# Kernel optimization log

Hardware: AMD Instinct MI355X
Metric: run time of the kernel (lower is better)

The kernel has to match this reference:

```python
import jax, jax.numpy as jnp
import numpy as np

N_E = 8192
E_DIM = 64
BETA = 0.25
N_TOKENS = 32768


def setup_inputs() -> dict:
    key = jax.random.key(0)
    k1, k2 = jax.random.split(key)
    x = jax.random.normal(k1, (N_TOKENS, E_DIM), dtype=jnp.float32)
    # nn.Embedding weight initialized uniform(-1/n_e, 1/n_e)
    codebook = jax.random.uniform(k2, (N_E, E_DIM), dtype=jnp.float32,
                                  minval=-1.0 / N_E, maxval=1.0 / N_E)
    return {"x": x, "codebook": codebook, "start": 0, "end": N_E, "use_sk": 0}


def reference(x, codebook, start, end, use_sk):
    # use_sk=0 -> argmin branch (sinkhorn branch calls external helper, not exercised)
    latent = x.reshape(-1, E_DIM)                       # [N, D]
    cb = codebook[start:end]                            # [K, D]
    # squared euclidean distances: ||z||^2 + ||e||^2 - 2 z.e
    d = (jnp.sum(latent * latent, axis=1, keepdims=True)
         + jnp.sum(cb * cb, axis=1)[None, :]
         - 2.0 * jnp.einsum('nd,kd->nk', latent, cb))   # [N, K]
    indices = jnp.argmin(d, axis=-1) + start            # [N]
    x_q = codebook[indices].reshape(x.shape)            # gather
    sg = jax.lax.stop_gradient
    commitment_loss = jnp.mean((sg(x_q) - x) ** 2)
    codebook_loss = jnp.mean((x_q - sg(x)) ** 2)
    loss = codebook_loss + BETA * commitment_loss
    x_q_st = x + sg(x_q - x)                            # straight-through estimator
    indices = indices.reshape(x.shape[:-1])
    return x_q_st, loss, indices
```

## Files before the change

kernel.cpp:

```cpp
#include <hip/hip_runtime.h>
#include <math.h>


#define N_E    8192
#define EDIM   64
#define NTOK   32768
#define NELEM  (NTOK * EDIM)
#define CSZ    32
#define NCHUNK (N_E / CSZ)
#define WINDOW 3e-4f
#define KEXT   80
#define TTOK   256
#define TCODE  2048
#define SROW   88

typedef __attribute__((ext_vector_type(8)))  short          short8;
typedef __attribute__((ext_vector_type(8)))  unsigned short ushort8v;
typedef __attribute__((ext_vector_type(4)))  unsigned short ushort4v;
typedef __attribute__((ext_vector_type(16))) float          f32x16;

__device__ __forceinline__ unsigned short f2bf(float f) {
  unsigned int u = __float_as_uint(f);
  return (unsigned short)((u + 0x7FFFu + ((u >> 16) & 1u)) >> 16);
}
__device__ __forceinline__ unsigned short f2h(float f) {
  union { _Float16 h; unsigned short u; } cv; cv.h = (_Float16)f; return cv.u;
}
__device__ __forceinline__ float h2f(unsigned short b) {
  union { _Float16 h; unsigned short u; } cv; cv.u = b; return (float)cv.h;
}

__global__ __launch_bounds__(256) void vq_sc(const float* __restrict__ cb,
                                             float* __restrict__ sc,
                                             unsigned short* __restrict__ cbf) {
#pragma clang fp contract(off)
  int r = blockIdx.x * 256 + threadIdx.x;
  const float4* c4 = (const float4*)(cb + (size_t)r * EDIM);
  float a[8];
#pragma unroll
  for (int j = 0; j < 8; ++j) a[j] = 0.0f;
#pragma unroll
  for (int i = 0; i < 8; ++i) {
    float4 pA = c4[2*i], pB = c4[2*i+1];
    a[0] += pA.x * pA.x; a[1] += pA.y * pA.y; a[2] += pA.z * pA.z; a[3] += pA.w * pA.w;
    a[4] += pB.x * pB.x; a[5] += pB.y * pB.y; a[6] += pB.z * pB.z; a[7] += pB.w * pB.w;
  }
  float sval = ((a[0]+a[1]) + (a[2]+a[3])) + ((a[4]+a[5]) + (a[6]+a[7]));
  sc[r] = sval;
  unsigned short* dst = cbf + (size_t)r * KEXT;
#pragma unroll
  for (int h = 0; h < 8; ++h) {
    float4 fA = c4[2*h], fB = c4[2*h+1];
    ushort8v o = {f2bf(fA.x), f2bf(fA.y), f2bf(fA.z), f2bf(fA.w),
                  f2bf(fB.x), f2bf(fB.y), f2bf(fB.z), f2bf(fB.w)};
    *(ushort8v*)&dst[h * 8] = o;
  }
  ushort8v t0 = {0,0,0,0,0,0,0,0};
  t0[0] = f2bf(sval);
  *(ushort8v*)&dst[64] = t0;
  ushort8v z = {0,0,0,0,0,0,0,0};
  *(ushort8v*)&dst[72] = z;
}

__global__ __launch_bounds__(256, 2) void vq_pass1(
    const float* __restrict__ x, const unsigned short* __restrict__ cbf,
    unsigned short* __restrict__ minima, unsigned int* __restrict__ maskb,
    const int* __restrict__ p_start, const int* __restrict__ p_end) {
  __shared__ unsigned short Xs[TTOK * SROW];
  __shared__ unsigned short Cs[128 * SROW];
  int tid = threadIdx.x;
  int tb = blockIdx.x;
  int cbk = blockIdx.y;
  int s = *p_start, e = *p_end;

  const float4* xg = (const float4*)(x + (size_t)tb * TTOK * EDIM);
#pragma unroll
  for (int p = 0; p < 16; ++p) {
    int idx = tid + p * 256;
    int row = idx >> 4, c4i = idx & 15;
    float4 f = xg[idx];
    ushort4v o = {f2bf(f.x), f2bf(f.y), f2bf(f.z), f2bf(f.w)};
    *(ushort4v*)&Xs[row * SROW + c4i * 4] = o;
  }
  {
    ushort8v t0 = {0,0,0,0,0,0,0,0};
    t0[0] = f2bf(-0.5f);
    ushort8v z = {0,0,0,0,0,0,0,0};
    *(ushort8v*)&Xs[tid * SROW + 64] = t0;
    *(ushort8v*)&Xs[tid * SROW + 72] = z;
  }
  const ushort8v* cg0 = (const ushort8v*)(cbf + (size_t)cbk * TCODE * KEXT);
#pragma unroll
  for (int p = 0; p < 5; ++p) {
    int idx = tid + p * 256;
    int row = idx / 10, h = idx % 10;
    *(ushort8v*)&Cs[row * SROW + h * 8] = cg0[idx];
  }
  __syncthreads();

  int lane = tid & 63, wv = tid >> 6;
  int half = lane >> 5, ln = lane & 31;
  int tokbase = wv * 64;
  short8 bfr[2][5];
#pragma unroll
  for (int tg = 0; tg < 2; ++tg)
#pragma unroll
    for (int ks = 0; ks < 5; ++ks)
      bfr[tg][ks] = *(const short8*)&Xs[(tokbase + tg*32 + ln) * SROW + ks*16 + half*8];

  for (int nb = 0; nb < 16; ++nb) {
    ushort8v creg[5];
    if (nb < 15) {
      const ushort8v* cg =
          (const ushort8v*)(cbf + ((size_t)cbk * TCODE + (nb + 1) * 128) * KEXT);
#pragma unroll
      for (int p = 0; p < 5; ++p) creg[p] = cg[tid + p * 256];
    }
    f32x16 acc[2][4];
#pragma unroll
    for (int tg = 0; tg < 2; ++tg)
#pragma unroll
      for (int ct = 0; ct < 4; ++ct) acc[tg][ct] = (f32x16)0.0f;
#pragma unroll
    for (int ks = 0; ks < 5; ++ks)
#pragma unroll
      for (int ct = 0; ct < 4; ++ct) {
        short8 a = *(const short8*)&Cs[(ct*32 + ln) * SROW + ks*16 + half*8];
        acc[0][ct] = __builtin_amdgcn_mfma_f32_32x32x16_bf16(a, bfr[0][ks],
                                                             acc[0][ct], 0, 0, 0);
        acc[1][ct] = __builtin_amdgcn_mfma_f32_32x32x16_bf16(a, bfr[1][ks],
                                                             acc[1][ct], 0, 0, 0);
      }
    __syncthreads();
    if (nb < 15) {
#pragma unroll
      for (int p = 0; p < 5; ++p) {
        int idx = tid + p * 256;
        int row = idx / 10, h = idx % 10;
        *(ushort8v*)&Cs[row * SROW + h * 8] = creg[p];
      }
    }
    int cbase0 = cbk * TCODE + nb * 128;
    float vmv[2][4];
    unsigned mbits[2][4];
#pragma unroll
    for (int ct = 0; ct < 4; ++ct) {
      int c0 = cbase0 + ct * 32;
      bool full = (c0 >= s) && (c0 + 32 <= e);
#pragma unroll
      for (int tg = 0; tg < 2; ++tg) {
        float v = -INFINITY;
        if (full) {
#pragma unroll
          for (int r = 0; r < 16; ++r) v = fmaxf(v, acc[tg][ct][r]);
        } else {
#pragma unroll
          for (int r = 0; r < 16; ++r) {
            int code = c0 + (r & 3) + 8 * (r >> 2) + 4 * half;
            if (code >= s && code < e) v = fmaxf(v, acc[tg][ct][r]);
          }
        }
        v = fmaxf(v, __shfl_xor(v, 32, 64));
        vmv[tg][ct] = v;
        float t = v - WINDOW * 0.5f;
        unsigned b = 0;
#pragma unroll
        for (int r = 0; r < 16; ++r) {
          int pos = (r & 3) + 8 * (r >> 2) + 4 * half;
          if (acc[tg][ct][r] >= t) b |= (1u << pos);
        }
        b |= __shfl_xor(b, 32, 64);
        mbits[tg][ct] = b;
      }
    }
    int token = tb * TTOK + tokbase + lane;
    uint2 pk;
    pk.x = (unsigned int)f2h(-2.0f * vmv[half][0])
         | ((unsigned int)f2h(-2.0f * vmv[half][1]) << 16);
    pk.y = (unsigned int)f2h(-2.0f * vmv[half][2])
         | ((unsigned int)f2h(-2.0f * vmv[half][3]) << 16);
    *(uint2*)(minima + (size_t)token * NCHUNK + (cbase0 >> 5)) = pk;
    uint4 mq;
    mq.x = mbits[half][0]; mq.y = mbits[half][1];
    mq.z = mbits[half][2]; mq.w = mbits[half][3];
    *(uint4*)(maskb + (size_t)token * NCHUNK + (cbase0 >> 5)) = mq;
    __syncthreads();
  }
}

__global__ __launch_bounds__(256) void vq_rescue(
    const float* __restrict__ x, const float* __restrict__ cb,
    const float* __restrict__ sc, const unsigned short* __restrict__ minima,
    const unsigned int* __restrict__ maskb,
    float* __restrict__ out_xq, float* __restrict__ out_idx,
    float* __restrict__ partial,
    const int* __restrict__ p_start, const int* __restrict__ p_end) {
#pragma clang fp contract(off)
  __shared__ float xs[4][64];
  __shared__ float sdata[4];
  int tid  = threadIdx.x;
  int wv   = tid >> 6;
  int lane = tid & 63;
  int token = blockIdx.x * 4 + wv;

  float xx = x[(size_t)token * EDIM + lane];
  xs[wv][lane] = xx;
  __syncthreads();
  const float4* xl4 = (const float4*)xs[wv];

  float a[8];
#pragma unroll
  for (int j = 0; j < 8; ++j) a[j] = 0.0f;
#pragma unroll
  for (int i = 0; i < 8; ++i) {
    float4 pA = xl4[2*i], pB = xl4[2*i+1];
    a[0] += pA.x * pA.x; a[1] += pA.y * pA.y; a[2] += pA.z * pA.z; a[3] += pA.w * pA.w;
    a[4] += pB.x * pB.x; a[5] += pB.y * pB.y; a[6] += pB.z * pB.z; a[7] += pB.w * pB.w;
  }
  float sx = ((a[0]+a[1]) + (a[2]+a[3])) + ((a[4]+a[5]) + (a[6]+a[7]));

  uint2 u2 = *(const uint2*)(minima + (size_t)token * NCHUNK + lane * 4);
  float mv[4] = {h2f((unsigned short)(u2.x & 0xFFFFu)),
                 h2f((unsigned short)(u2.x >> 16)),
                 h2f((unsigned short)(u2.y & 0xFFFFu)),
                 h2f((unsigned short)(u2.y >> 16))};
  float m = fminf(fminf(mv[0], mv[1]), fminf(mv[2], mv[3]));
#pragma unroll
  for (int off = 32; off >= 1; off >>= 1) m = fminf(m, __shfl_xor(m, off, 64));
  float thr = m + WINDOW;

  int s = *p_start, e = *p_end;
  unsigned long long bestpack = ~0ull;

  bool anyf = (mv[0] <= thr) | (mv[1] <= thr) | (mv[2] <= thr) | (mv[3] <= thr);
  if (anyf) {
    uint4 mq = *(const uint4*)(maskb + (size_t)token * NCHUNK + lane * 4);
    unsigned mks[4] = {mq.x, mq.y, mq.z, mq.w};
#pragma unroll 1
    for (int cc = 0; cc < 4; ++cc) {
      if (!(mv[cc] <= thr)) continue;
      unsigned msk = mks[cc];
      while (msk) {
        int j = __ffs(msk) - 1;
        msk &= msk - 1;
        int k = (lane * 4 + cc) * CSZ + j;
        if (k >= s && k < e) {
          const float4* c4 = (const float4*)(cb + (size_t)k * EDIM);
          float t[8];
#pragma unroll
          for (int jj = 0; jj < 8; ++jj) t[jj] = 0.0f;
#pragma unroll
          for (int i = 0; i < 8; ++i) {
            float4 cA4 = c4[2*i], cB4 = c4[2*i+1];
            float4 pA = xl4[2*i], pB = xl4[2*i+1];
            t[0] += cA4.x * pA.x; t[1] += cA4.y * pA.y;
            t[2] += cA4.z * pA.z; t[3] += cA4.w * pA.w;
            t[4] += cB4.x * pB.x; t[5] += cB4.y * pB.y;
            t[6] += cB4.z * pB.z; t[7] += cB4.w * pB.w;
          }
          float tt = ((t[0]+t[1]) + (t[2]+t[3])) + ((t[4]+t[5]) + (t[6]+t[7]));
          float d = (sx + sc[k]) - 2.0f * tt;
          unsigned int db = __float_as_uint(d);
          unsigned int en = db ^ ((unsigned int)((int)db >> 31) | 0x80000000u);
          unsigned long long pk = ((unsigned long long)en << 32) | (unsigned int)k;
          if (pk < bestpack) bestpack = pk;
        }
      }
    }
  }
#pragma unroll
  for (int off = 32; off >= 1; off >>= 1) {
    unsigned long long o = __shfl_xor(bestpack, off, 64);
    if (o < bestpack) bestpack = o;
  }
  int bidx = (int)(unsigned int)(bestpack & 0xFFFFFFFFull);

  float qv = cb[(size_t)bidx * EDIM + lane];
  float diff = qv - xx;
  out_xq[(size_t)token * EDIM + lane] = xx + diff;
  if (lane == 0) out_idx[token] = (float)bidx;

  float l = diff * diff;
#pragma unroll
  for (int off = 32; off >= 1; off >>= 1) l += __shfl_down(l, off, 64);
  if (lane == 0) sdata[wv] = l;
  __syncthreads();
  if (tid == 0)
    partial[blockIdx.x] = (sdata[0] + sdata[1]) + (sdata[2] + sdata[3]);
}

__global__ __launch_bounds__(256) void vq_loss(const float* __restrict__ partial,
                                               float* __restrict__ out_loss) {
  int tid = threadIdx.x;
  float s = 0.0f;
  for (int i = tid; i < NTOK / 4; i += 256) s += partial[i];
#pragma unroll
  for (int off = 32; off >= 1; off >>= 1) s += __shfl_down(s, off, 64);
  __shared__ float sdata[4];
  if ((tid & 63) == 0) sdata[tid >> 6] = s;
  __syncthreads();
  if (tid == 0) {
    float total = (sdata[0] + sdata[1]) + (sdata[2] + sdata[3]);
    float m = total * (1.0f / (float)NELEM);
    out_loss[0] = m + 0.25f * m;
  }
}

extern "C" void kernel_launch(void* const* d_in, const int* in_sizes, int n_in,
                              void* d_out, int out_size, void* d_ws, size_t ws_size,
                              hipStream_t stream) {
  const float* x  = (const float*)d_in[0];
  const float* cb = (const float*)d_in[1];
  const int* p_start = (const int*)d_in[2];
  const int* p_end   = (const int*)d_in[3];

  float* ws = (float*)d_ws;
  float* sc      = ws;
  float* partial = ws + N_E;
  unsigned short* cbf    = (unsigned short*)(ws + 2 * N_E);
  unsigned short* minima = cbf + (size_t)N_E * KEXT;
  unsigned int*   maskb  = (unsigned int*)(minima + (size_t)NTOK * NCHUNK);

  float* out      = (float*)d_out;
  float* out_xq   = out;
  float* out_loss = out + NELEM;
  float* out_idx  = out + NELEM + 1;

  vq_sc<<<N_E / 256, 256, 0, stream>>>(cb, sc, cbf);
  dim3 g1(NTOK / TTOK, N_E / TCODE);
  vq_pass1<<<g1, 256, 0, stream>>>(x, cbf, minima, maskb, p_start, p_end);
  vq_rescue<<<NTOK / 4, 256, 0, stream>>>(x, cb, sc, minima, maskb, out_xq, out_idx,
                                          partial, p_start, p_end);
  vq_loss<<<1, 256, 0, stream>>>(partial, out_loss);
}
```

Baseline: 213.3 us.

## Replace per-chunk minima and bitmasks with compact per-token candidate lists

The first pass no longer writes a half-precision minimum and a 32-bit mask for every 32-code chunk of every token. Instead it keeps a running maximum per token across each 2048-code block and records up to 14 candidate code indices that fall within the window, writing one fixed 32-byte record per token per block. The rescue kernel then evaluates each token's candidates in exact fp32 across wave lanes in parallel. If a block overflows its slots, it falls back to a brute-force scan of that whole 2048-code block. This removes most of the intermediate global-memory write and read traffic, at the cost of extra shared-memory list building and occasional expensive overflow scans.

```diff
diff --git a/kernel.cpp b/kernel.cpp
--- a/kernel.cpp
+++ b/kernel.cpp
@@ -6,13 +6,13 @@
 #define EDIM   64
 #define NTOK   32768
 #define NELEM  (NTOK * EDIM)
-#define CSZ    32
-#define NCHUNK (N_E / CSZ)
 #define WINDOW 3e-4f
+#define AWIN   1.5e-4f
 #define KEXT   80
 #define TTOK   256
 #define TCODE  2048
 #define SROW   88
+#define SLOTS  14
 
 typedef __attribute__((ext_vector_type(8)))  short          short8;
 typedef __attribute__((ext_vector_type(8)))  unsigned short ushort8v;
@@ -23,11 +23,29 @@
   unsigned int u = __float_as_uint(f);
   return (unsigned short)((u + 0x7FFFu + ((u >> 16) & 1u)) >> 16);
 }
-__device__ __forceinline__ unsigned short f2h(float f) {
-  union { _Float16 h; unsigned short u; } cv; cv.h = (_Float16)f; return cv.u;
-}
-__device__ __forceinline__ float h2f(unsigned short b) {
-  union { _Float16 h; unsigned short u; } cv; cv.u = b; return (float)cv.h;
+
+__device__ __forceinline__ unsigned long long vq_eval_pack(
+    const float* __restrict__ cb, int k, const float4* __restrict__ xl4,
+    float sx, const float* __restrict__ sc) {
+#pragma clang fp contract(off)
+  const float4* c4 = (const float4*)(cb + (size_t)k * EDIM);
+  float t[8];
+#pragma unroll
+  for (int j = 0; j < 8; ++j) t[j] = 0.0f;
+#pragma unroll
+  for (int i = 0; i < 8; ++i) {
+    float4 cA4 = c4[2*i], cB4 = c4[2*i+1];
+    float4 pA = xl4[2*i], pB = xl4[2*i+1];
+    t[0] += cA4.x * pA.x; t[1] += cA4.y * pA.y;
+    t[2] += cA4.z * pA.z; t[3] += cA4.w * pA.w;
+    t[4] += cB4.x * pB.x; t[5] += cB4.y * pB.y;
+    t[6] += cB4.z * pB.z; t[7] += cB4.w * pB.w;
+  }
+  float tt = ((t[0]+t[1]) + (t[2]+t[3])) + ((t[4]+t[5]) + (t[6]+t[7]));
+  float d = (sx + sc[k]) - 2.0f * tt;
+  unsigned int db = __float_as_uint(d);
+  unsigned int en = db ^ ((unsigned int)((int)db >> 31) | 0x80000000u);
+  return ((unsigned long long)en << 32) | (unsigned int)k;
 }
 
 __global__ __launch_bounds__(256) void vq_sc(const float* __restrict__ cb,
@@ -64,10 +82,11 @@
 
 __global__ __launch_bounds__(256, 2) void vq_pass1(
     const float* __restrict__ x, const unsigned short* __restrict__ cbf,
-    unsigned short* __restrict__ minima, unsigned int* __restrict__ maskb,
+    unsigned int* __restrict__ cand,
     const int* __restrict__ p_start, const int* __restrict__ p_end) {
   __shared__ unsigned short Xs[TTOK * SROW];
   __shared__ unsigned short Cs[128 * SROW];
+  __shared__ unsigned short cl[TTOK][16];
   int tid = threadIdx.x;
   int tb = blockIdx.x;
   int cbk = blockIdx.y;
@@ -108,6 +127,9 @@
     for (int ks = 0; ks < 5; ++ks)
       bfr[tg][ks] = *(const short8*)&Xs[(tokbase + tg*32 + ln) * SROW + ks*16 + half*8];
 
+  float runmax[2] = {-INFINITY, -INFINITY};
+  int cnt = 0;
+
   for (int nb = 0; nb < 16; ++nb) {
     ushort8v creg[5];
     if (nb < 15) {
@@ -141,57 +163,78 @@
       }
     }
     int cbase0 = cbk * TCODE + nb * 128;
-    float vmv[2][4];
-    unsigned mbits[2][4];
+    bool full = (cbase0 >= s) && (cbase0 + 128 <= e);
+    float rm0 = -INFINITY, rm1 = -INFINITY;
+    if (full) {
+#pragma unroll
+      for (int ct = 0; ct < 4; ++ct)
+#pragma unroll
+        for (int r = 0; r < 16; ++r) {
+          rm0 = fmaxf(rm0, acc[0][ct][r]);
+          rm1 = fmaxf(rm1, acc[1][ct][r]);
+        }
+    } else {
+#pragma unroll
+      for (int ct = 0; ct < 4; ++ct)
+#pragma unroll
+        for (int r = 0; r < 16; ++r) {
+          int code = cbase0 + ct * 32 + (r & 3) + 8 * (r >> 2) + 4 * half;
+          if (code >= s && code < e) {
+            rm0 = fmaxf(rm0, acc[0][ct][r]);
+            rm1 = fmaxf(rm1, acc[1][ct][r]);
+          }
+        }
+    }
+    rm0 = fmaxf(rm0, __shfl_xor(rm0, 32, 64));
+    rm1 = fmaxf(rm1, __shfl_xor(rm1, 32, 64));
+    runmax[0] = fmaxf(runmax[0], rm0);
+    runmax[1] = fmaxf(runmax[1], rm1);
+    float t0 = runmax[0] - AWIN, t1 = runmax[1] - AWIN;
 #pragma unroll
     for (int ct = 0; ct < 4; ++ct) {
       int c0 = cbase0 + ct * 32;
-      bool full = (c0 >= s) && (c0 + 32 <= e);
-#pragma unroll
-      for (int tg = 0; tg < 2; ++tg) {
-        float v = -INFINITY;
-        if (full) {
-#pragma unroll
-          for (int r = 0; r < 16; ++r) v = fmaxf(v, acc[tg][ct][r]);
-        } else {
-#pragma unroll
-          for (int r = 0; r < 16; ++r) {
-            int code = c0 + (r & 3) + 8 * (r >> 2) + 4 * half;
-            if (code >= s && code < e) v = fmaxf(v, acc[tg][ct][r]);
-          }
-        }
-        v = fmaxf(v, __shfl_xor(v, 32, 64));
-        vmv[tg][ct] = v;
-        float t = v - WINDOW * 0.5f;
-        unsigned b = 0;
+      unsigned b0 = 0, b1 = 0;
+      if (full) {
 #pragma unroll
         for (int r = 0; r < 16; ++r) {
           int pos = (r & 3) + 8 * (r >> 2) + 4 * half;
-          if (acc[tg][ct][r] >= t) b |= (1u << pos);
+          if (acc[0][ct][r] >= t0) b0 |= (1u << pos);
+          if (acc[1][ct][r] >= t1) b1 |= (1u << pos);
         }
-        b |= __shfl_xor(b, 32, 64);
-        mbits[tg][ct] = b;
-      }
-    }
-    int token = tb * TTOK + tokbase + lane;
-    uint2 pk;
-    pk.x = (unsigned int)f2h(-2.0f * vmv[half][0])
-         | ((unsigned int)f2h(-2.0f * vmv[half][1]) << 16);
-    pk.y = (unsigned int)f2h(-2.0f * vmv[half][2])
-         | ((unsigned int)f2h(-2.0f * vmv[half][3]) << 16);
-    *(uint2*)(minima + (size_t)token * NCHUNK + (cbase0 >> 5)) = pk;
-    uint4 mq;
-    mq.x = mbits[half][0]; mq.y = mbits[half][1];
-    mq.z = mbits[half][2]; mq.w = mbits[half][3];
-    *(uint4*)(maskb + (size_t)token * NCHUNK + (cbase0 >> 5)) = mq;
+      } else {
+#pragma unroll
+        for (int r = 0; r < 16; ++r) {
+          int pos = (r & 3) + 8 * (r >> 2) + 4 * half;
+          bool ok = (c0 + pos >= s) && (c0 + pos < e);
+          if (ok && acc[0][ct][r] >= t0) b0 |= (1u << pos);
+          if (ok && acc[1][ct][r] >= t1) b1 |= (1u << pos);
+        }
+      }
+      b0 |= __shfl_xor(b0, 32, 64);
+      b1 |= __shfl_xor(b1, 32, 64);
+      unsigned m = half ? b1 : b0;
+      while (m) {
+        int j = __ffs(m) - 1;
+        m &= m - 1;
+        if (cnt < SLOTS) cl[tid][cnt] = (unsigned short)(c0 + j);
+        ++cnt;
+      }
+    }
     __syncthreads();
   }
+  int token = tb * TTOK + tid;
+  const unsigned* clu = (const unsigned*)cl[tid];
+  uint4 w0, w1;
+  w0.x = (unsigned)cnt; w0.y = clu[0]; w0.z = clu[1]; w0.w = clu[2];
+  w1.x = clu[3]; w1.y = clu[4]; w1.z = clu[5]; w1.w = clu[6];
+  unsigned* rec = cand + ((size_t)cbk * NTOK + token) * 8;
+  *(uint4*)rec = w0;
+  *(uint4*)(rec + 4) = w1;
 }
 
 __global__ __launch_bounds__(256) void vq_rescue(
     const float* __restrict__ x, const float* __restrict__ cb,
-    const float* __restrict__ sc, const unsigned short* __restrict__ minima,
-    const unsigned int* __restrict__ maskb,
+    const float* __restrict__ sc, const unsigned int* __restrict__ cand,
     float* __restrict__ out_xq, float* __restrict__ out_idx,
     float* __restrict__ partial,
     const int* __restrict__ p_start, const int* __restrict__ p_end) {
@@ -219,52 +262,27 @@
   }
   float sx = ((a[0]+a[1]) + (a[2]+a[3])) + ((a[4]+a[5]) + (a[6]+a[7]));
 
-  uint2 u2 = *(const uint2*)(minima + (size_t)token * NCHUNK + lane * 4);
-  float mv[4] = {h2f((unsigned short)(u2.x & 0xFFFFu)),
-                 h2f((unsigned short)(u2.x >> 16)),
-                 h2f((unsigned short)(u2.y & 0xFFFFu)),
-                 h2f((unsigned short)(u2.y >> 16))};
-  float m = fminf(fminf(mv[0], mv[1]), fminf(mv[2], mv[3]));
-#pragma unroll
-  for (int off = 32; off >= 1; off >>= 1) m = fminf(m, __shfl_xor(m, off, 64));
-  float thr = m + WINDOW;
-
   int s = *p_start, e = *p_end;
   unsigned long long bestpack = ~0ull;
 
-  bool anyf = (mv[0] <= thr) | (mv[1] <= thr) | (mv[2] <= thr) | (mv[3] <= thr);
-  if (anyf) {
-    uint4 mq = *(const uint4*)(maskb + (size_t)token * NCHUNK + lane * 4);
-    unsigned mks[4] = {mq.x, mq.y, mq.z, mq.w};
+  int b = lane >> 4, slot = lane & 15;
+  const unsigned* rec = cand + ((size_t)b * NTOK + token) * 8;
+  unsigned cnt = rec[0];
+  if (cnt <= SLOTS && slot < (int)cnt) {
+    int k = (int)((rec[1 + (slot >> 1)] >> ((slot & 1) * 16)) & 0xFFFFu);
+    unsigned long long pk = vq_eval_pack(cb, k, xl4, sx, sc);
+    if (pk < bestpack) bestpack = pk;
+  }
+  unsigned long long ovf = __ballot(slot == 0 && cnt > SLOTS);
+  while (ovf) {
+    int ob = (__ffsll((long long)ovf) - 1) >> 4;
+    ovf &= ovf - 1;
 #pragma unroll 1
-    for (int cc = 0; cc < 4; ++cc) {
-      if (!(mv[cc] <= thr)) continue;
-      unsigned msk = mks[cc];
-      while (msk) {
-        int j = __ffs(msk) - 1;
-        msk &= msk - 1;
-        int k = (lane * 4 + cc) * CSZ + j;
-        if (k >= s && k < e) {
-          const float4* c4 = (const float4*)(cb + (size_t)k * EDIM);
-          float t[8];
-#pragma unroll
-          for (int jj = 0; jj < 8; ++jj) t[jj] = 0.0f;
-#pragma unroll
-          for (int i = 0; i < 8; ++i) {
-            float4 cA4 = c4[2*i], cB4 = c4[2*i+1];
-            float4 pA = xl4[2*i], pB = xl4[2*i+1];
-            t[0] += cA4.x * pA.x; t[1] += cA4.y * pA.y;
-            t[2] += cA4.z * pA.z; t[3] += cA4.w * pA.w;
-            t[4] += cB4.x * pB.x; t[5] += cB4.y * pB.y;
-            t[6] += cB4.z * pB.z; t[7] += cB4.w * pB.w;
-          }
-          float tt = ((t[0]+t[1]) + (t[2]+t[3])) + ((t[4]+t[5]) + (t[6]+t[7]));
-          float d = (sx + sc[k]) - 2.0f * tt;
-          unsigned int db = __float_as_uint(d);
-          unsigned int en = db ^ ((unsigned int)((int)db >> 31) | 0x80000000u);
-          unsigned long long pk = ((unsigned long long)en << 32) | (unsigned int)k;
-          if (pk < bestpack) bestpack = pk;
-        }
+    for (int r = 0; r < TCODE / 64; ++r) {
+      int k = ob * TCODE + r * 64 + lane;
+      if (k >= s && k < e) {
+        unsigned long long pk = vq_eval_pack(cb, k, xl4, sx, sc);
+        if (pk < bestpack) bestpack = pk;
       }
     }
   }
@@ -317,9 +335,8 @@
   float* ws = (float*)d_ws;
   float* sc      = ws;
   float* partial = ws + N_E;
-  unsigned short* cbf    = (unsigned short*)(ws + 2 * N_E);
-  unsigned short* minima = cbf + (size_t)N_E * KEXT;
-  unsigned int*   maskb  = (unsigned int*)(minima + (size_t)NTOK * NCHUNK);
+  unsigned short* cbf = (unsigned short*)(ws + 2 * N_E);
+  unsigned int*   cand = (unsigned int*)(cbf + (size_t)N_E * KEXT);
 
   float* out      = (float*)d_out;
   float* out_xq   = out;
@@ -328,8 +345,8 @@
 
   vq_sc<<<N_E / 256, 256, 0, stream>>>(cb, sc, cbf);
   dim3 g1(NTOK / TTOK, N_E / TCODE);
-  vq_pass1<<<g1, 256, 0, stream>>>(x, cbf, minima, maskb, p_start, p_end);
-  vq_rescue<<<NTOK / 4, 256, 0, stream>>>(x, cb, sc, minima, maskb, out_xq, out_idx,
+  vq_pass1<<<g1, 256, 0, stream>>>(x, cbf, cand, p_start, p_end);
+  vq_rescue<<<NTOK / 4, 256, 0, stream>>>(x, cb, sc, cand, out_xq, out_idx,
                                           partial, p_start, p_end);
   vq_loss<<<1, 256, 0, stream>>>(partial, out_loss);
 }
```

Result: slower. 713.2 us (+234.3%).

## Drop per-code candidate bitmasks; rescue checks whole flagged chunks lane-parallel

Applied to the files above, without the earlier changes.

Pass1 stops building and writing the per-token 32-bit candidate masks and only writes chunk minima, now batched into 16-byte stores covering four iterations. The rescue kernel no longer reads masks. It ballots the flagged chunks and evaluates every code in each flagged chunk, one code per lane, two chunks per wave pass. This removes mask compute and a large global write/read stream, but rescue does exact fp32 work on all 32 codes of every flagged chunk rather than only the masked ones.

```diff
diff --git a/kernel.cpp b/kernel.cpp
--- a/kernel.cpp
+++ b/kernel.cpp
@@ -30,6 +30,30 @@
   union { _Float16 h; unsigned short u; } cv; cv.u = b; return (float)cv.h;
 }
 
+__device__ __forceinline__ unsigned long long vq_eval_pack(
+    const float* __restrict__ cb, int k, const float4* __restrict__ xl4,
+    float sx, const float* __restrict__ sc) {
+#pragma clang fp contract(off)
+  const float4* c4 = (const float4*)(cb + (size_t)k * EDIM);
+  float t[8];
+#pragma unroll
+  for (int j = 0; j < 8; ++j) t[j] = 0.0f;
+#pragma unroll
+  for (int i = 0; i < 8; ++i) {
+    float4 cA4 = c4[2*i], cB4 = c4[2*i+1];
+    float4 pA = xl4[2*i], pB = xl4[2*i+1];
+    t[0] += cA4.x * pA.x; t[1] += cA4.y * pA.y;
+    t[2] += cA4.z * pA.z; t[3] += cA4.w * pA.w;
+    t[4] += cB4.x * pB.x; t[5] += cB4.y * pB.y;
+    t[6] += cB4.z * pB.z; t[7] += cB4.w * pB.w;
+  }
+  float tt = ((t[0]+t[1]) + (t[2]+t[3])) + ((t[4]+t[5]) + (t[6]+t[7]));
+  float d = (sx + sc[k]) - 2.0f * tt;
+  unsigned int db = __float_as_uint(d);
+  unsigned int en = db ^ ((unsigned int)((int)db >> 31) | 0x80000000u);
+  return ((unsigned long long)en << 32) | (unsigned int)k;
+}
+
 __global__ __launch_bounds__(256) void vq_sc(const float* __restrict__ cb,
                                              float* __restrict__ sc,
                                              unsigned short* __restrict__ cbf) {
@@ -64,7 +88,7 @@
 
 __global__ __launch_bounds__(256, 2) void vq_pass1(
     const float* __restrict__ x, const unsigned short* __restrict__ cbf,
-    unsigned short* __restrict__ minima, unsigned int* __restrict__ maskb,
+    unsigned short* __restrict__ minima,
     const int* __restrict__ p_start, const int* __restrict__ p_end) {
   __shared__ unsigned short Xs[TTOK * SROW];
   __shared__ unsigned short Cs[128 * SROW];
@@ -108,90 +132,89 @@
     for (int ks = 0; ks < 5; ++ks)
       bfr[tg][ks] = *(const short8*)&Xs[(tokbase + tg*32 + ln) * SROW + ks*16 + half*8];
 
-  for (int nb = 0; nb < 16; ++nb) {
-    ushort8v creg[5];
-    if (nb < 15) {
-      const ushort8v* cg =
-          (const ushort8v*)(cbf + ((size_t)cbk * TCODE + (nb + 1) * 128) * KEXT);
-#pragma unroll
-      for (int p = 0; p < 5; ++p) creg[p] = cg[tid + p * 256];
-    }
-    f32x16 acc[2][4];
-#pragma unroll
-    for (int tg = 0; tg < 2; ++tg)
-#pragma unroll
-      for (int ct = 0; ct < 4; ++ct) acc[tg][ct] = (f32x16)0.0f;
-#pragma unroll
-    for (int ks = 0; ks < 5; ++ks)
+  int token = tb * TTOK + tokbase + lane;
+  unsigned short* rowp = minima + (size_t)token * NCHUNK + cbk * 64;
+
+  for (int nbg = 0; nbg < 4; ++nbg) {
+    unsigned pk8[8];
+#pragma unroll
+    for (int ni = 0; ni < 4; ++ni) {
+      int nb = nbg * 4 + ni;
+      ushort8v creg[5];
+      if (nb < 15) {
+        const ushort8v* cg =
+            (const ushort8v*)(cbf + ((size_t)cbk * TCODE + (nb + 1) * 128) * KEXT);
+#pragma unroll
+        for (int p = 0; p < 5; ++p) creg[p] = cg[tid + p * 256];
+      }
+      f32x16 acc[2][4];
+#pragma unroll
+      for (int tg = 0; tg < 2; ++tg)
+#pragma unroll
+        for (int ct = 0; ct < 4; ++ct) acc[tg][ct] = (f32x16)0.0f;
+#pragma unroll
+      for (int ks = 0; ks < 5; ++ks)
+#pragma unroll
+        for (int ct = 0; ct < 4; ++ct) {
+          short8 a = *(const short8*)&Cs[(ct*32 + ln) * SROW + ks*16 + half*8];
+          acc[0][ct] = __builtin_amdgcn_mfma_f32_32x32x16_bf16(a, bfr[0][ks],
+                                                               acc[0][ct], 0, 0, 0);
+          acc[1][ct] = __builtin_amdgcn_mfma_f32_32x32x16_bf16(a, bfr[1][ks],
+                                                               acc[1][ct], 0, 0, 0);
+        }
+      __syncthreads();
+      if (nb < 15) {
+#pragma unroll
+        for (int p = 0; p < 5; ++p) {
+          int idx = tid + p * 256;
+          int row = idx / 10, h = idx % 10;
+          *(ushort8v*)&Cs[row * SROW + h * 8] = creg[p];
+        }
+      }
+      int cbase0 = cbk * TCODE + nb * 128;
+      bool full = (cbase0 >= s) && (cbase0 + 128 <= e);
+      float cm[4];
 #pragma unroll
       for (int ct = 0; ct < 4; ++ct) {
-        short8 a = *(const short8*)&Cs[(ct*32 + ln) * SROW + ks*16 + half*8];
-        acc[0][ct] = __builtin_amdgcn_mfma_f32_32x32x16_bf16(a, bfr[0][ks],
-                                                             acc[0][ct], 0, 0, 0);
-        acc[1][ct] = __builtin_amdgcn_mfma_f32_32x32x16_bf16(a, bfr[1][ks],
-                                                             acc[1][ct], 0, 0, 0);
-      }
-    __syncthreads();
-    if (nb < 15) {
-#pragma unroll
-      for (int p = 0; p < 5; ++p) {
-        int idx = tid + p * 256;
-        int row = idx / 10, h = idx % 10;
-        *(ushort8v*)&Cs[row * SROW + h * 8] = creg[p];
-      }
-    }
-    int cbase0 = cbk * TCODE + nb * 128;
-    float vmv[2][4];
-    unsigned mbits[2][4];
-#pragma unroll
-    for (int ct = 0; ct < 4; ++ct) {
-      int c0 = cbase0 + ct * 32;
-      bool full = (c0 >= s) && (c0 + 32 <= e);
-#pragma unroll
-      for (int tg = 0; tg < 2; ++tg) {
-        float v = -INFINITY;
+        float v0 = -INFINITY, v1 = -INFINITY;
         if (full) {
 #pragma unroll
-          for (int r = 0; r < 16; ++r) v = fmaxf(v, acc[tg][ct][r]);
+          for (int r = 0; r < 16; ++r) {
+            v0 = fmaxf(v0, acc[0][ct][r]);
+            v1 = fmaxf(v1, acc[1][ct][r]);
+          }
         } else {
+          int c0 = cbase0 + ct * 32;
 #pragma unroll
           for (int r = 0; r < 16; ++r) {
             int code = c0 + (r & 3) + 8 * (r >> 2) + 4 * half;
-            if (code >= s && code < e) v = fmaxf(v, acc[tg][ct][r]);
+            if (code >= s && code < e) {
+              v0 = fmaxf(v0, acc[0][ct][r]);
+              v1 = fmaxf(v1, acc[1][ct][r]);
+            }
           }
         }
-        v = fmaxf(v, __shfl_xor(v, 32, 64));
-        vmv[tg][ct] = v;
-        float t = v - WINDOW * 0.5f;
-        unsigned b = 0;
-#pragma unroll
-        for (int r = 0; r < 16; ++r) {
-          int pos = (r & 3) + 8 * (r >> 2) + 4 * half;
-          if (acc[tg][ct][r] >= t) b |= (1u << pos);
-        }
-        b |= __shfl_xor(b, 32, 64);
-        mbits[tg][ct] = b;
-      }
+        v0 = fmaxf(v0, __shfl_xor(v0, 32, 64));
+        v1 = fmaxf(v1, __shfl_xor(v1, 32, 64));
+        cm[ct] = half ? v1 : v0;
+      }
+      pk8[ni*2]     = (unsigned)f2h(-2.0f * cm[0])
+                    | ((unsigned)f2h(-2.0f * cm[1]) << 16);
+      pk8[ni*2 + 1] = (unsigned)f2h(-2.0f * cm[2])
+                    | ((unsigned)f2h(-2.0f * cm[3]) << 16);
+      __syncthreads();
     }
-    int token = tb * TTOK + tokbase + lane;
-    uint2 pk;
-    pk.x = (unsigned int)f2h(-2.0f * vmv[half][0])
-         | ((unsigned int)f2h(-2.0f * vmv[half][1]) << 16);
-    pk.y = (unsigned int)f2h(-2.0f * vmv[half][2])
-         | ((unsigned int)f2h(-2.0f * vmv[half][3]) << 16);
-    *(uint2*)(minima + (size_t)token * NCHUNK + (cbase0 >> 5)) = pk;
-    uint4 mq;
-    mq.x = mbits[half][0]; mq.y = mbits[half][1];
-    mq.z = mbits[half][2]; mq.w = mbits[half][3];
-    *(uint4*)(maskb + (size_t)token * NCHUNK + (cbase0 >> 5)) = mq;
-    __syncthreads();
+    uint4 w0, w1;
+    w0.x = pk8[0]; w0.y = pk8[1]; w0.z = pk8[2]; w0.w = pk8[3];
+    w1.x = pk8[4]; w1.y = pk8[5]; w1.z = pk8[6]; w1.w = pk8[7];
+    *(uint4*)(rowp + nbg * 16)     = w0;
+    *(uint4*)(rowp + nbg * 16 + 8) = w1;
   }
 }
 
 __global__ __launch_bounds__(256) void vq_rescue(
     const float* __restrict__ x, const float* __restrict__ cb,
     const float* __restrict__ sc, const unsigned short* __restrict__ minima,
-    const unsigned int* __restrict__ maskb,
     float* __restrict__ out_xq, float* __restrict__ out_idx,
     float* __restrict__ partial,
     const int* __restrict__ p_start, const int* __restrict__ p_end) {
@@ -228,44 +251,36 @@
 #pragma unroll
   for (int off = 32; off >= 1; off >>= 1) m = fminf(m, __shfl_xor(m, off, 64));
   float thr = m + WINDOW;
+  unsigned long long fmask[4];
+#pragma unroll
+  for (int cc = 0; cc < 4; ++cc) fmask[cc] = __ballot(mv[cc] <= thr);
 
   int s = *p_start, e = *p_end;
   unsigned long long bestpack = ~0ull;
-
-  bool anyf = (mv[0] <= thr) | (mv[1] <= thr) | (mv[2] <= thr) | (mv[3] <= thr);
-  if (anyf) {
-    uint4 mq = *(const uint4*)(maskb + (size_t)token * NCHUNK + lane * 4);
-    unsigned mks[4] = {mq.x, mq.y, mq.z, mq.w};
+  int half = lane >> 5;
+  int pend = -1;
+
 #pragma unroll 1
-    for (int cc = 0; cc < 4; ++cc) {
-      if (!(mv[cc] <= thr)) continue;
-      unsigned msk = mks[cc];
-      while (msk) {
-        int j = __ffs(msk) - 1;
-        msk &= msk - 1;
-        int k = (lane * 4 + cc) * CSZ + j;
+  for (int cc = 0; cc < 5; ++cc) {
+    unsigned long long fm = (cc < 4) ? fmask[cc] : 0ull;
+    while (fm || (cc == 4 && pend >= 0)) {
+      int cA, cB;
+      if (cc == 4) { cA = pend; cB = -1; pend = -2; }
+      else {
+        int b = __ffsll((long long)fm) - 1; fm &= fm - 1;
+        int c = b * 4 + cc;
+        if (pend < 0) { pend = c; continue; }
+        cA = pend; cB = c; pend = -1;
+      }
+      int ch = half ? cB : cA;
+      if (ch >= 0) {
+        int k = ch * CSZ + (lane & 31);
         if (k >= s && k < e) {
-          const float4* c4 = (const float4*)(cb + (size_t)k * EDIM);
-          float t[8];
-#pragma unroll
-          for (int jj = 0; jj < 8; ++jj) t[jj] = 0.0f;
-#pragma unroll
-          for (int i = 0; i < 8; ++i) {
-            float4 cA4 = c4[2*i], cB4 = c4[2*i+1];
-            float4 pA = xl4[2*i], pB = xl4[2*i+1];
-            t[0] += cA4.x * pA.x; t[1] += cA4.y * pA.y;
-            t[2] += cA4.z * pA.z; t[3] += cA4.w * pA.w;
-            t[4] += cB4.x * pB.x; t[5] += cB4.y * pB.y;
-            t[6] += cB4.z * pB.z; t[7] += cB4.w * pB.w;
-          }
-          float tt = ((t[0]+t[1]) + (t[2]+t[3])) + ((t[4]+t[5]) + (t[6]+t[7]));
-          float d = (sx + sc[k]) - 2.0f * tt;
-          unsigned int db = __float_as_uint(d);
-          unsigned int en = db ^ ((unsigned int)((int)db >> 31) | 0x80000000u);
-          unsigned long long pk = ((unsigned long long)en << 32) | (unsigned int)k;
+          unsigned long long pk = vq_eval_pack(cb, k, xl4, sx, sc);
           if (pk < bestpack) bestpack = pk;
         }
       }
+      if (pend == -2) { pend = -1; break; }
     }
   }
 #pragma unroll
@@ -317,9 +332,8 @@
   float* ws = (float*)d_ws;
   float* sc      = ws;
   float* partial = ws + N_E;
-  unsigned short* cbf    = (unsigned short*)(ws + 2 * N_E);
+  unsigned short* cbf = (unsigned short*)(ws + 2 * N_E);
   unsigned short* minima = cbf + (size_t)N_E * KEXT;
-  unsigned int*   maskb  = (unsigned int*)(minima + (size_t)NTOK * NCHUNK);
 
   float* out      = (float*)d_out;
   float* out_xq   = out;
@@ -328,8 +342,8 @@
 
   vq_sc<<<N_E / 256, 256, 0, stream>>>(cb, sc, cbf);
   dim3 g1(NTOK / TTOK, N_E / TCODE);
-  vq_pass1<<<g1, 256, 0, stream>>>(x, cbf, minima, maskb, p_start, p_end);
-  vq_rescue<<<NTOK / 4, 256, 0, stream>>>(x, cb, sc, minima, maskb, out_xq, out_idx,
+  vq_pass1<<<g1, 256, 0, stream>>>(x, cbf, minima, p_start, p_end);
+  vq_rescue<<<NTOK / 4, 256, 0, stream>>>(x, cb, sc, minima, out_xq, out_idx,
                                           partial, p_start, p_end);
   vq_loss<<<1, 256, 0, stream>>>(partial, out_loss);
 }
```

Measured after the change: 219.0 us. 2.6% more time.
